# Kernel tuning notes

Measured on AMD Instinct MI355X. Metric: run time of the kernel, lower is better.

## Reference

```python
import jax, jax.numpy as jnp
import numpy as np

CLUSTERS = 128
ITERATIONS = 10
TOPK = 32
NEG = -1e7


def setup_inputs() -> dict:
    key = jax.random.key(0)
    k1, k2, k3, k4 = jax.random.split(key, 4)
    N, L, H, E = 2, 2048, 8, 64
    BITS = 32
    return {
        "queries": jax.random.normal(k1, (N, L, H, E), dtype=jnp.float32),
        "keys": jax.random.normal(k2, (N, L, H, E), dtype=jnp.float32),
        "values": jax.random.normal(k3, (N, L, H, E), dtype=jnp.float32),
        "planes": jax.random.normal(k4, (BITS, E + 1), dtype=jnp.float32),
    }


def _cluster(bits, C, iterations):
    # bits: [N,H,L,B] in {0,1}. Lloyd k-means under Hamming distance.
    N, H, L, B = bits.shape
    init_idx = (np.arange(C) * L) // C
    cent = bits[:, :, init_idx, :]  # [N,H,C,B]
    for _ in range(iterations):
        # hamming(b,c) = b.(1-c) + (1-b).c
        d = (jnp.einsum('nhlb,nhcb->nhlc', bits, 1.0 - cent)
             + jnp.einsum('nhlb,nhcb->nhlc', 1.0 - bits, cent))
        assign = jnp.argmin(d, axis=-1)                      # [N,H,L]
        oh = jax.nn.one_hot(assign, C, dtype=jnp.float32)    # [N,H,L,C]
        cnt = oh.sum(axis=2)                                 # [N,H,C]
        sums = jnp.einsum('nhlc,nhlb->nhcb', oh, bits)
        new = (sums / jnp.maximum(cnt, 1.0)[..., None] >= 0.5).astype(jnp.float32)
        cent = jnp.where((cnt > 0.0)[..., None], new, cent)
    d = (jnp.einsum('nhlb,nhcb->nhlc', bits, 1.0 - cent)
         + jnp.einsum('nhlb,nhcb->nhlc', 1.0 - bits, cent))
    assign = jnp.argmin(d, axis=-1)
    oh = jax.nn.one_hot(assign, C, dtype=jnp.float32)
    cnt = oh.sum(axis=2)
    return assign, oh, cnt


def _forward(queries, keys, values, planes):
    # to [N,H,L,E]
    Q = jnp.transpose(queries, (0, 2, 1, 3))
    K = jnp.transpose(keys, (0, 2, 1, 3))
    V = jnp.transpose(values, (0, 2, 1, 3))
    N, H, L, E = Q.shape
    S = K.shape[2]
    temp = 1.0 / np.sqrt(E)

    # --- hash queries with random hyperplanes (bias column: hash_bias=True) ---
    x = jnp.concatenate([Q, jnp.ones(Q.shape[:-1] + (1,), Q.dtype)], axis=-1)
    bits = (jnp.einsum('nhle,be->nhlb', x, planes) > 0).astype(jnp.float32)

    # --- cluster queries (Lloyd on hamming distance over hash bits) ---
    assign, oh, cnt = _cluster(bits, CLUSTERS, ITERATIONS)

    # --- per-cluster centroid queries (mean over members) ---
    Qg = jnp.einsum('nhlc,nhle->nhce', oh, Q) / jnp.maximum(cnt, 1.0)[..., None]

    # --- top-k keys per cluster ---
    QKc = jnp.einsum('nhce,nhse->nhcs', Qg, K)   # [N,H,C,S]
    k = min(TOPK, S)
    _, tki = jax.lax.top_k(QKc, k)               # [N,H,C,k]

    # broadcast each cluster's top-k indices to its member queries
    idx_q = jnp.take_along_axis(
        tki, jnp.broadcast_to(assign[:, :, :, None], (N, H, L, k)), axis=2)  # [N,H,L,k]

    gather = jax.vmap(jax.vmap(lambda a, i: a[i]))
    K_sel = gather(K, idx_q)                     # [N,H,L,k,E]
    V_sel = gather(V, idx_q)                     # [N,H,L,k,E]

    qk = jnp.einsum('nhle,nhlke->nhlk', Q, K_sel)
    future = idx_q > jnp.arange(L)[None, None, :, None]   # causal: key pos > query pos
    qk = jnp.where(future, NEG, qk)
    A = jax.nn.softmax(temp * qk, axis=-1)
    A = A * (1.0 - future.astype(A.dtype))
    out = jnp.einsum('nhlk,nhlkd->nhld', A, V_sel)
    return jnp.transpose(out, (0, 2, 1, 3))      # [N,L,H,D]


def reference(queries, keys, values, planes):
    return _forward(queries, keys, values, planes)
```

## Files before the change

kernel.cpp:

```cpp
#include <hip/hip_runtime.h>
#include <math.h>

#define NB 2
#define HB 8
#define LB 2048
#define EB 64
#define BITSN 32
#define CLN 128
#define ITERS 10
#define TOPKN 32
#define NEGV -10000000.0f

typedef unsigned long long u64;
typedef unsigned int u32;

#define PART_NH16 (33 * 64)
#define PART_ITER16 (NB * HB * PART_NH16)
#define PART_TOTAL16 (ITERS * PART_ITER16)
#define BITS_BLOCKS 4096
#define ZBLOCKS ((PART_TOTAL16 + 255) / 256)

__global__ __launch_bounds__(256) void bits_zero_kernel(const float* __restrict__ q,
                                                        const float* __restrict__ planes,
                                                        u32* __restrict__ bits,
                                                        u32* __restrict__ zbuf) {
    int tid = threadIdx.x;
    int bid = blockIdx.x;
    if (bid >= BITS_BLOCKS) {
        int i = (bid - BITS_BLOCKS) * 256 + tid;
        if (i < PART_TOTAL16) zbuf[i] = 0u;
        return;
    }
    int wave = tid >> 6;
    int lane = tid & 63;
    int b = lane & 31;
    int which = lane >> 5;
    int qi = bid * 8 + wave * 2 + which;
    int l = qi & (LB - 1);
    int nh = qi / LB;
    int h = nh & (HB - 1);
    int n = nh / HB;
    const float* qrow = q + (((long long)n * LB + l) * HB + h) * EB;
    const float* prow = planes + b * (EB + 1);
    double acc = (double)prow[EB];
    #pragma unroll 8
    for (int e = 0; e < EB; ++e) acc += (double)qrow[e] * (double)prow[e];
    unsigned long long m = __ballot(acc > 0.0);
    if (b == 0) {
        bits[qi] = (u32)(which ? (m >> 32) : (m & 0xffffffffULL));
    }
}

__global__ __launch_bounds__(256) void kmeans_iter_kernel(const u32* __restrict__ bits,
                                                          const u32* __restrict__ part_prev,
                                                          u32* __restrict__ part_cur,
                                                          const u32* __restrict__ cent_prev_g,
                                                          u32* __restrict__ cent_cur_g,
                                                          int it) {
    __shared__ u32 cent[CLN];
    __shared__ int hist[33 * 128];
    int tid = threadIdx.x;
    int bid = blockIdx.x;
    int nh = bid >> 3;
    int tile = bid & 7;
    int lane = tid & 63;

    for (int i = tid; i < 33 * 128; i += 256) hist[i] = 0;
    if (tid < CLN) {
        u32 cv;
        if (it == 0) {
            cv = bits[nh * LB + tid * (LB / CLN)];
        } else {
            const u32* pp = part_prev + nh * PART_NH16;
            int sh = (tid & 1) * 16;
            int cnt = (int)((pp[32 * 64 + (tid >> 1)] >> sh) & 0xffffu);
            u32 nb = 0u;
            #pragma unroll
            for (int j = 0; j < BITSN; ++j) {
                int s = (int)((pp[j * 64 + (tid >> 1)] >> sh) & 0xffffu);
                if (2 * s >= cnt) nb |= (1u << j);
            }
            cv = (cnt > 0) ? nb : cent_prev_g[nh * CLN + tid];
        }
        cent[tid] = cv;
        if (tile == 0) cent_cur_g[nh * CLN + tid] = cv;
    }
    __syncthreads();

    int l = tile * 256 + tid;
    u32 bv = bits[nh * LB + l];

    u32 clo = cent[lane], chi = cent[lane + 64];
    u32 best = 0x7fffffffu;
    #pragma unroll 16
    for (int c = 0; c < 64; ++c) {
        u32 cc = (u32)__builtin_amdgcn_readlane((int)clo, c);
        u32 key = ((u32)__popc(bv ^ cc) << 7) | (u32)c;
        best = (key < best) ? key : best;
    }
    #pragma unroll 16
    for (int c = 0; c < 64; ++c) {
        u32 cc = (u32)__builtin_amdgcn_readlane((int)chi, c);
        u32 key = ((u32)__popc(bv ^ cc) << 7) | (u32)(64 + c);
        best = (key < best) ? key : best;
    }
    int bc = (int)(best & 127u);

    atomicAdd(&hist[32 * 128 + bc], 1);
    u32 bb = bv;
    while (bb) { int j = __ffs(bb) - 1; atomicAdd(&hist[j * 128 + bc], 1); bb &= bb - 1; }
    __syncthreads();

    u32* pc = part_cur + nh * PART_NH16;
    for (int i = tid; i < PART_NH16; i += 256) {
        int j = i >> 6, p = i & 63;
        u32 v = (u32)hist[j * 128 + 2 * p] | ((u32)hist[j * 128 + 2 * p + 1] << 16);
        if (v) atomicAdd(&pc[i], v);
    }
}

__global__ __launch_bounds__(1024) void list_qg_final_kernel(const u32* __restrict__ bits,
                                                             const u32* __restrict__ part_prev,
                                                             const u32* __restrict__ cent_prev_g,
                                                             const float* __restrict__ q,
                                                             int* __restrict__ cnt_g,
                                                             int* __restrict__ ofs_g,
                                                             int* __restrict__ list_g,
                                                             float* __restrict__ qgf) {
    __shared__ u32 cent[CLN];
    __shared__ int cnt[CLN];
    __shared__ int cntw[2][16][CLN];
    __shared__ int ofs[CLN];
    __shared__ unsigned short lists[LB];
    int nh = blockIdx.x;
    int tid = threadIdx.x;
    int w = tid >> 6, lane = tid & 63;

    if (tid < CLN) {
        const u32* pp = part_prev + nh * PART_NH16;
        int sh = (tid & 1) * 16;
        int cn = (int)((pp[32 * 64 + (tid >> 1)] >> sh) & 0xffffu);
        u32 nb = 0u;
        #pragma unroll
        for (int j = 0; j < BITSN; ++j) {
            int s = (int)((pp[j * 64 + (tid >> 1)] >> sh) & 0xffffu);
            if (2 * s >= cn) nb |= (1u << j);
        }
        cent[tid] = (cn > 0) ? nb : cent_prev_g[nh * CLN + tid];
        cnt[tid] = 0;
    }
    for (int i = tid; i < 2 * 16 * CLN; i += 1024) (&cntw[0][0][0])[i] = 0;
    __syncthreads();

    int l0 = tid, l1 = tid + 1024;
    u32 bv0 = bits[nh * LB + l0];
    u32 bv1 = bits[nh * LB + l1];
    u32 clo = cent[lane], chi = cent[lane + 64];
    u32 best0 = 0x7fffffffu, best1 = 0x7fffffffu;
    #pragma unroll 16
    for (int c = 0; c < 64; ++c) {
        u32 cc = (u32)__builtin_amdgcn_readlane((int)clo, c);
        u32 k0 = ((u32)__popc(bv0 ^ cc) << 7) | (u32)c;
        u32 k1 = ((u32)__popc(bv1 ^ cc) << 7) | (u32)c;
        best0 = (k0 < best0) ? k0 : best0;
        best1 = (k1 < best1) ? k1 : best1;
    }
    #pragma unroll 16
    for (int c = 0; c < 64; ++c) {
        u32 cc = (u32)__builtin_amdgcn_readlane((int)chi, c);
        u32 k0 = ((u32)__popc(bv0 ^ cc) << 7) | (u32)(64 + c);
        u32 k1 = ((u32)__popc(bv1 ^ cc) << 7) | (u32)(64 + c);
        best0 = (k0 < best0) ? k0 : best0;
        best1 = (k1 < best1) ? k1 : best1;
    }
    int bc0 = (int)(best0 & 127u);
    int bc1 = (int)(best1 & 127u);
    u64 ltmask = (lane == 0) ? 0ULL : (~0ULL >> (64 - lane));

    int rank0 = 0, rank1 = 0;
    for (int c = 0; c < CLN; ++c) {
        u64 m0 = __ballot(bc0 == c);
        u64 m1 = __ballot(bc1 == c);
        if ((m0 | m1) == 0ULL) continue;
        if (bc0 == c) rank0 = (int)__popcll(m0 & ltmask);
        if (bc1 == c) rank1 = (int)__popcll(m1 & ltmask);
        if (lane == 0) {
            int p0 = (int)__popcll(m0), p1 = (int)__popcll(m1);
            if (p0) cntw[0][w][c] = p0;
            if (p1) cntw[1][w][c] = p1;
            atomicAdd(&cnt[c], p0 + p1);
        }
    }
    __syncthreads();
    if (tid == 0) {
        int run = 0;
        for (int c = 0; c < CLN; ++c) { ofs[c] = run; run += cnt[c]; }
    }
    __syncthreads();
    if (tid < CLN) {
        int c = tid;
        int run = ofs[c];
        #pragma unroll
        for (int g = 0; g < 2; ++g)
            for (int ww = 0; ww < 16; ++ww) {
                int t = cntw[g][ww][c];
                cntw[g][ww][c] = run;
                run += t;
            }
        cnt_g[nh * CLN + c] = cnt[c];
        ofs_g[nh * CLN + c] = ofs[c];
    }
    __syncthreads();
    {
        int p0 = cntw[0][w][bc0] + rank0;
        int p1 = cntw[1][w][bc1] + rank1;
        lists[p0] = (unsigned short)l0;
        lists[p1] = (unsigned short)l1;
        list_g[nh * LB + p0] = l0;
        list_g[nh * LB + p1] = l1;
    }
    __syncthreads();

    int h = nh & (HB - 1);
    int n = nh / HB;
    for (int c = w; c < CLN; c += 16) {
        int cn = cnt[c];
        int o = ofs[c];
        double acc = 0.0;
        for (int i = 0; i < cn; ++i) {
            int l = lists[o + i];
            acc += (double)q[(((long long)n * LB + l) * HB + h) * EB + lane];
        }
        double dcn = (double)(cn > 0 ? cn : 1);
        qgf[(long long)(nh * CLN + c) * EB + lane] = (float)(acc / dcn);
    }
}

__global__ __launch_bounds__(256) void scores_kernel(const float* __restrict__ kk,
                                                     const float* __restrict__ qgf,
                                                     u32* __restrict__ keys) {
    int bid = blockIdx.x;
    int nh = bid >> 4;
    int tile = bid & 15;
    int h = nh & (HB - 1);
    int n = nh / HB;
    int w = threadIdx.x >> 6;
    int lane = threadIdx.x & 63;
    int rl = (w & 1) * 64 + lane;
    int l = tile * 128 + rl;
    int cbase = (w >> 1) * 64;

    const float4* kr4 = (const float4*)(kk + (((long long)n * LB + l) * HB + h) * EB);
    float rr[EB];
    #pragma unroll
    for (int i = 0; i < 16; ++i) {
        float4 t4 = kr4[i];
        rr[4 * i] = t4.x; rr[4 * i + 1] = t4.y; rr[4 * i + 2] = t4.z; rr[4 * i + 3] = t4.w;
    }
    const float* qp0 = qgf + ((long long)nh * CLN + cbase) * EB;
    for (int c = 0; c < 64; ++c) {
        const float4* qp = (const float4*)(qp0 + c * EB);
        float acc = 0.f;
        #pragma unroll
        for (int i = 0; i < 16; ++i) {
            float4 qv = qp[i];
            acc = fmaf(qv.x, rr[4 * i], acc);
            acc = fmaf(qv.y, rr[4 * i + 1], acc);
            acc = fmaf(qv.z, rr[4 * i + 2], acc);
            acc = fmaf(qv.w, rr[4 * i + 3], acc);
        }
        u32 u = __float_as_uint(acc);
        u = ((int)u < 0) ? ~u : (u | 0x80000000u);
        keys[((long long)(nh * CLN + cbase + c)) * LB + l] = u;
    }
}

__global__ __launch_bounds__(256) void topsel_attn_kernel(const u32* __restrict__ keys,
                                                          const float* __restrict__ q,
                                                          const float* __restrict__ kk,
                                                          const float* __restrict__ vv,
                                                          const int* __restrict__ cnt_g,
                                                          const int* __restrict__ ofs_g,
                                                          const int* __restrict__ list_g,
                                                          float* __restrict__ out) {
    __shared__ int tki_s[TOPKN];
    __shared__ float ks[TOPKN][EB + 1];
    __shared__ float vs[TOPKN][EB];
    int bid = blockIdx.x;
    int nh = bid >> 7;
    int h = nh & (HB - 1);
    int n = nh / HB;
    int tid = threadIdx.x;
    int cnt = cnt_g[bid];
    if (cnt == 0) return;
    int o = ofs_g[bid];
    int wave = tid >> 6, lane = tid & 63;

    if (tid < 64) {
        const uint4* kp4 = (const uint4*)(keys + (long long)bid * LB);
        u64 k[32];
        #pragma unroll
        for (int t = 0; t < 8; ++t) {
            uint4 kv = kp4[lane + 64 * t];
            int l0 = (lane + 64 * t) * 4;
            k[4 * t]     = ((u64)kv.x << 32) | (u32)(2047 - l0);
            k[4 * t + 1] = ((u64)kv.y << 32) | (u32)(2047 - (l0 + 1));
            k[4 * t + 2] = ((u64)kv.z << 32) | (u32)(2047 - (l0 + 2));
            k[4 * t + 3] = ((u64)kv.w << 32) | (u32)(2047 - (l0 + 3));
        }
        u64 m0 = k[0], m1 = k[8], m2 = k[16], m3 = k[24];
        #pragma unroll
        for (int t = 1; t < 8; ++t) {
            if (k[t] > m0) m0 = k[t];
            if (k[8 + t] > m1) m1 = k[8 + t];
            if (k[16 + t] > m2) m2 = k[16 + t];
            if (k[24 + t] > m3) m3 = k[24 + t];
        }
        if (m1 > m0) m0 = m1;
        if (m3 > m2) m2 = m3;
        u64 cur = (m2 > m0) ? m2 : m0;
        for (int r = 0; r < TOPKN; ++r) {
            u64 wk = cur;
            #pragma unroll
            for (int off = 1; off < 64; off <<= 1) {
                u64 oo = __shfl_xor(wk, off);
                if (oo > wk) wk = oo;
            }
            if (lane == 0) tki_s[r] = 2047 - (int)(wk & 2047u);
            if (wk == cur) {
                u64 nm = 0ULL;
                #pragma unroll
                for (int t = 0; t < 32; ++t) {
                    u64 kt = k[t];
                    u64 cand = (kt < wk) ? kt : 0ULL;
                    if (cand > nm) nm = cand;
                }
                cur = nm;
            }
        }
    }
    __syncthreads();

    {
        int r = tid >> 3, seg = tid & 7;
        int kr = tki_s[r];
        const float* krow = kk + (((long long)n * LB + kr) * HB + h) * EB + seg * 8;
        const float* vrow = vv + (((long long)n * LB + kr) * HB + h) * EB + seg * 8;
        float4 a0 = ((const float4*)krow)[0], a1 = ((const float4*)krow)[1];
        float4 b0 = ((const float4*)vrow)[0], b1 = ((const float4*)vrow)[1];
        int e0 = seg * 8;
        ks[r][e0 + 0] = a0.x; ks[r][e0 + 1] = a0.y; ks[r][e0 + 2] = a0.z; ks[r][e0 + 3] = a0.w;
        ks[r][e0 + 4] = a1.x; ks[r][e0 + 5] = a1.y; ks[r][e0 + 6] = a1.z; ks[r][e0 + 7] = a1.w;
        ((float4*)&vs[r][e0])[0] = b0;
        ((float4*)&vs[r][e0])[1] = b1;
    }
    __syncthreads();

    for (int i = wave; i < cnt; i += 4) {
        int l = list_g[nh * LB + o + i];
        int j = lane & 31, p = lane >> 5;
        int kidx = tki_s[j];

        const float4* q4 = (const float4*)(q + (((long long)n * LB + l) * HB + h) * EB) + p * 8;
        float part = 0.f;
        #pragma unroll
        for (int i4 = 0; i4 < 8; ++i4) {
            float4 a = q4[i4];
            int e0 = p * 32 + i4 * 4;
            part += a.x * ks[j][e0] + a.y * ks[j][e0 + 1] + a.z * ks[j][e0 + 2] + a.w * ks[j][e0 + 3];
        }
        float qlo = __shfl(part, j);
        float qhi = __shfl(part, j + 32);
        float qk = qlo + qhi;

        bool future = kidx > l;
        float logit = 0.125f * (future ? NEGV : qk);
        float m = logit;
        #pragma unroll
        for (int off = 16; off; off >>= 1) m = fmaxf(m, __shfl_xor(m, off));
        float ex = expf(logit - m);
        float ssum = ex;
        #pragma unroll
        for (int off = 16; off; off >>= 1) ssum += __shfl_xor(ssum, off);
        float a = future ? 0.f : ex / ssum;

        float oacc = 0.f;
        #pragma unroll
        for (int jj = 0; jj < TOPKN; ++jj) {
            float aj = __shfl(a, jj);
            oacc = fmaf(aj, vs[jj][lane], oacc);
        }
        out[(((long long)n * LB + l) * HB + h) * EB + lane] = oacc;
    }
}

extern "C" void kernel_launch(void* const* d_in, const int* in_sizes, int n_in,
                              void* d_out, int out_size, void* d_ws, size_t ws_size,
                              hipStream_t stream) {
    const float* q = (const float*)d_in[0];
    const float* k = (const float*)d_in[1];
    const float* v = (const float*)d_in[2];
    const float* planes = (const float*)d_in[3];
    float* out = (float*)d_out;

    char* ws = (char*)d_ws;
    u32* bits     = (u32*)(ws);
    int* cnt_g    = (int*)(ws + 0x40000);
    int* ofs_g    = (int*)(ws + 0x42000);
    int* list_g   = (int*)(ws + 0x44000);
    float* qgf    = (float*)(ws + 0x64000);
    u32* keys     = (u32*)(ws + 0x124000);
    u32* part_all = (u32*)(ws + 0x124000);
    u32* cents0   = (u32*)(ws + 0x124000 + 0x180000);
    u32* cents1   = (u32*)(ws + 0x124000 + 0x182000);

    bits_zero_kernel<<<BITS_BLOCKS + ZBLOCKS, 256, 0, stream>>>(q, planes, bits, part_all);

    for (int it = 0; it < ITERS; ++it) {
        const u32* pp = part_all + (it == 0 ? 0 : (it - 1)) * PART_ITER16;
        u32* pc       = part_all + it * PART_ITER16;
        const u32* cprev = (it & 1) ? cents0 : cents1;
        u32* ccur        = (it & 1) ? cents1 : cents0;
        kmeans_iter_kernel<<<NB * HB * 8, 256, 0, stream>>>(bits, pp, pc, cprev, ccur, it);
    }
    list_qg_final_kernel<<<NB * HB, 1024, 0, stream>>>(
        bits, part_all + 9 * PART_ITER16, cents1, q, cnt_g, ofs_g, list_g, qgf);
    scores_kernel<<<NB * HB * 16, 256, 0, stream>>>(k, qgf, keys);
    topsel_attn_kernel<<<NB * HB * CLN, 256, 0, stream>>>(keys, q, k, v,
                                                          cnt_g, ofs_g, list_g, out);
}
```

Measured before the change: 293.1 us.

## Split top-k selection from attention and chunk cluster members across blocks

New measurement: 347.0 us. 1.18x slower.

```diff
diff --git a/kernel.cpp b/kernel.cpp
--- a/kernel.cpp
+++ b/kernel.cpp
@@ -10,6 +10,7 @@
 #define ITERS 10
 #define TOPKN 32
 #define NEGV -10000000.0f
+#define NCH 4
 
 typedef unsigned long long u64;
 typedef unsigned int u32;
@@ -275,70 +276,80 @@
     }
 }
 
-__global__ __launch_bounds__(256) void topsel_attn_kernel(const u32* __restrict__ keys,
-                                                          const float* __restrict__ q,
-                                                          const float* __restrict__ kk,
-                                                          const float* __restrict__ vv,
-                                                          const int* __restrict__ cnt_g,
-                                                          const int* __restrict__ ofs_g,
-                                                          const int* __restrict__ list_g,
-                                                          float* __restrict__ out) {
+__global__ __launch_bounds__(64) void topsel_kernel(const u32* __restrict__ keys,
+                                                    int* __restrict__ tki_g) {
+    int bid = blockIdx.x;
+    int lane = threadIdx.x;
+    const uint4* kp4 = (const uint4*)(keys + (long long)bid * LB);
+    u64 k[32];
+    #pragma unroll
+    for (int t = 0; t < 8; ++t) {
+        uint4 kv = kp4[lane + 64 * t];
+        int l0 = (lane + 64 * t) * 4;
+        k[4 * t]     = ((u64)kv.x << 32) | (u32)(2047 - l0);
+        k[4 * t + 1] = ((u64)kv.y << 32) | (u32)(2047 - (l0 + 1));
+        k[4 * t + 2] = ((u64)kv.z << 32) | (u32)(2047 - (l0 + 2));
+        k[4 * t + 3] = ((u64)kv.w << 32) | (u32)(2047 - (l0 + 3));
+    }
+    u64 m0 = k[0], m1 = k[8], m2 = k[16], m3 = k[24];
+    #pragma unroll
+    for (int t = 1; t < 8; ++t) {
+        if (k[t] > m0) m0 = k[t];
+        if (k[8 + t] > m1) m1 = k[8 + t];
+        if (k[16 + t] > m2) m2 = k[16 + t];
+        if (k[24 + t] > m3) m3 = k[24 + t];
+    }
+    if (m1 > m0) m0 = m1;
+    if (m3 > m2) m2 = m3;
+    u64 cur = (m2 > m0) ? m2 : m0;
+
+    for (int r = 0; r < TOPKN; ++r) {
+        u64 wk = cur;
+        #pragma unroll
+        for (int off = 1; off < 64; off <<= 1) {
+            u64 o = __shfl_xor(wk, off);
+            if (o > wk) wk = o;
+        }
+        if (lane == 0) tki_g[bid * TOPKN + r] = 2047 - (int)(wk & 2047u);
+        if (wk == cur) {
+            u64 nm = 0ULL;
+            #pragma unroll
+            for (int t = 0; t < 32; ++t) {
+                u64 kt = k[t];
+                u64 cand = (kt < wk) ? kt : 0ULL;
+                if (cand > nm) nm = cand;
+            }
+            cur = nm;
+        }
+    }
+}
+
+__global__ __launch_bounds__(256) void attn_chunk_kernel(const int* __restrict__ tki_g,
+                                                         const float* __restrict__ q,
+                                                         const float* __restrict__ kk,
+                                                         const float* __restrict__ vv,
+                                                         const int* __restrict__ cnt_g,
+                                                         const int* __restrict__ ofs_g,
+                                                         const int* __restrict__ list_g,
+                                                         float* __restrict__ out) {
     __shared__ int tki_s[TOPKN];
     __shared__ float ks[TOPKN][EB + 1];
     __shared__ float vs[TOPKN][EB];
     int bid = blockIdx.x;
-    int nh = bid >> 7;
+    int chunk = bid & (NCH - 1);
+    int cidx = bid >> 2;
+    int nh = cidx >> 7;
     int h = nh & (HB - 1);
     int n = nh / HB;
     int tid = threadIdx.x;
-    int cnt = cnt_g[bid];
-    if (cnt == 0) return;
-    int o = ofs_g[bid];
+    int cnt = cnt_g[cidx];
+    int base = chunk * 64;
+    if (base >= cnt) return;
+    int endq = (chunk == NCH - 1) ? cnt : ((cnt < base + 64) ? cnt : base + 64);
+    int o = ofs_g[cidx];
     int wave = tid >> 6, lane = tid & 63;
 
-    if (tid < 64) {
-        const uint4* kp4 = (const uint4*)(keys + (long long)bid * LB);
-        u64 k[32];
-        #pragma unroll
-        for (int t = 0; t < 8; ++t) {
-            uint4 kv = kp4[lane + 64 * t];
-            int l0 = (lane + 64 * t) * 4;
-            k[4 * t]     = ((u64)kv.x << 32) | (u32)(2047 - l0);
-            k[4 * t + 1] = ((u64)kv.y << 32) | (u32)(2047 - (l0 + 1));
-            k[4 * t + 2] = ((u64)kv.z << 32) | (u32)(2047 - (l0 + 2));
-            k[4 * t + 3] = ((u64)kv.w << 32) | (u32)(2047 - (l0 + 3));
-        }
-        u64 m0 = k[0], m1 = k[8], m2 = k[16], m3 = k[24];
-        #pragma unroll
-        for (int t = 1; t < 8; ++t) {
-            if (k[t] > m0) m0 = k[t];
-            if (k[8 + t] > m1) m1 = k[8 + t];
-            if (k[16 + t] > m2) m2 = k[16 + t];
-            if (k[24 + t] > m3) m3 = k[24 + t];
-        }
-        if (m1 > m0) m0 = m1;
-        if (m3 > m2) m2 = m3;
-        u64 cur = (m2 > m0) ? m2 : m0;
-        for (int r = 0; r < TOPKN; ++r) {
-            u64 wk = cur;
-            #pragma unroll
-            for (int off = 1; off < 64; off <<= 1) {
-                u64 oo = __shfl_xor(wk, off);
-                if (oo > wk) wk = oo;
-            }
-            if (lane == 0) tki_s[r] = 2047 - (int)(wk & 2047u);
-            if (wk == cur) {
-                u64 nm = 0ULL;
-                #pragma unroll
-                for (int t = 0; t < 32; ++t) {
-                    u64 kt = k[t];
-                    u64 cand = (kt < wk) ? kt : 0ULL;
-                    if (cand > nm) nm = cand;
-                }
-                cur = nm;
-            }
-        }
-    }
+    if (tid < TOPKN) tki_s[tid] = tki_g[cidx * TOPKN + tid];
     __syncthreads();
 
     {
@@ -356,7 +367,7 @@
     }
     __syncthreads();
 
-    for (int i = wave; i < cnt; i += 4) {
+    for (int i = base + wave; i < endq; i += 4) {
         int l = list_g[nh * LB + o + i];
         int j = lane & 31, p = lane >> 5;
         int kidx = tki_s[j];
@@ -409,6 +420,7 @@
     int* ofs_g    = (int*)(ws + 0x42000);
     int* list_g   = (int*)(ws + 0x44000);
     float* qgf    = (float*)(ws + 0x64000);
+    int* tki_g    = (int*)(ws + 0xE4000);
     u32* keys     = (u32*)(ws + 0x124000);
     u32* part_all = (u32*)(ws + 0x124000);
     u32* cents0   = (u32*)(ws + 0x124000 + 0x180000);
@@ -426,6 +438,7 @@
     list_qg_final_kernel<<<NB * HB, 1024, 0, stream>>>(
         bits, part_all + 9 * PART_ITER16, cents1, q, cnt_g, ofs_g, list_g, qgf);
     scores_kernel<<<NB * HB * 16, 256, 0, stream>>>(k, qgf, keys);
-    topsel_attn_kernel<<<NB * HB * CLN, 256, 0, stream>>>(keys, q, k, v,
-                                                          cnt_g, ofs_g, list_g, out);
-}
+    topsel_kernel<<<NB * HB * CLN, 64, 0, stream>>>(keys, tki_g);
+    attn_chunk_kernel<<<NB * HB * CLN * NCH, 256, 0, stream>>>(tki_g, q, k, v,
+                                                               cnt_g, ofs_g, list_g, out);
+}
```
